# Performance work log

Hardware: AMD Instinct MI355X
Metric: run time of the kernel (lower is better)

## Reference

```python
import jax, jax.numpy as jnp
import numpy as np

B, SEQ, F = 256, 2048, 5
IN1, U1, U2 = SEQ * F, 32, 1
UNFOLDS = 6          # ODE solver unfolds per cell call
ELAPSED = 1.0        # elapsed time per call


def _cell_params(key, n_in, n_u):
    ks = jax.random.split(key, 9)
    U = lambda k, shp, lo, hi: jax.random.uniform(k, shp, jnp.float32, lo, hi)
    return dict(
        input_w=jnp.ones((n_in,), jnp.float32),
        input_b=jnp.zeros((n_in,), jnp.float32),
        smu=U(ks[0], (n_in, n_u), 0.3, 0.8),
        ssig=U(ks[1], (n_in, n_u), 3.0, 8.0),
        sW=U(ks[2], (n_in, n_u), 0.001, 1.0),
        serev=2.0 * jax.random.bernoulli(ks[3], 0.5, (n_in, n_u)).astype(jnp.float32) - 1.0,
        mu=U(ks[4], (n_u, n_u), 0.3, 0.8),
        sig=U(ks[5], (n_u, n_u), 3.0, 8.0),
        W=U(ks[6], (n_u, n_u), 0.001, 1.0),
        erev=2.0 * jax.random.bernoulli(ks[7], 0.5, (n_u, n_u)).astype(jnp.float32) - 1.0,
        gleak=jnp.ones((n_u,), jnp.float32),
        vleak=U(ks[8], (n_u,), -0.2, 0.2),
        cm=0.5 * jnp.ones((n_u,), jnp.float32),
    )


def setup_inputs() -> dict:
    key = jax.random.key(0)
    kx, ka, kb = jax.random.split(key, 3)
    inp = {"x": jax.random.normal(kx, (B, SEQ, F), jnp.float32)}
    for pfx, k, n_in, n_u in (("a_", ka, IN1, U1), ("b_", kb, U1, U2)):
        for name, v in _cell_params(k, n_in, n_u).items():
            inp[pfx + name] = v
    return inp


def _ltc(x, iw, ib, smu, ssig, sW, serev, mu, sig, W, erev, gleak, vleak, cm):
    # x: [B, n_in]; input affine mapping
    x = x * iw + ib
    # sensory synapse activations: [B, n_in, n_u]
    sact = sW * jax.nn.sigmoid((x[:, :, None] - smu) * ssig)
    w_num_s = jnp.einsum('biu,iu->bu', sact, serev)   # reversal-weighted sum
    w_den_s = jnp.sum(sact, axis=1)
    cm_t = cm / (ELAPSED / UNFOLDS)                   # [n_u]
    v0 = jnp.zeros((x.shape[0], cm.shape[0]), x.dtype)

    def body(v, _):
        # recurrent synapses: presyn axis 1, postsyn axis 2 -> [B, n_u, n_u]
        wact = W * jax.nn.sigmoid((v[:, :, None] - mu) * sig)
        num = cm_t * v + gleak * vleak + jnp.einsum('bij,ij->bj', wact, erev) + w_num_s
        den = cm_t + gleak + jnp.sum(wact, axis=1) + w_den_s
        return num / den, None

    v, _ = jax.lax.scan(body, v0, None, length=UNFOLDS)
    return v


def reference(x,
              a_input_w, a_input_b, a_smu, a_ssig, a_sW, a_serev,
              a_mu, a_sig, a_W, a_erev, a_gleak, a_vleak, a_cm,
              b_input_w, b_input_b, b_smu, b_ssig, b_sW, b_serev,
              b_mu, b_sig, b_W, b_erev, b_gleak, b_vleak, b_cm):
    bsz = x.shape[0]
    xb = x.reshape(bsz, -1)  # [B, seq*5]
    h = _ltc(xb, a_input_w, a_input_b, a_smu, a_ssig, a_sW, a_serev,
             a_mu, a_sig, a_W, a_erev, a_gleak, a_vleak, a_cm)     # [B, 32]
    h2 = _ltc(h, b_input_w, b_input_b, b_smu, b_ssig, b_sW, b_serev,
              b_mu, b_sig, b_W, b_erev, b_gleak, b_vleak, b_cm)    # [B, 1]
    return jax.nn.sigmoid(h2).reshape(bsz)
```

## Files before the change

### kernel.cpp

```cpp
#include <hip/hip_runtime.h>

#define BATCH 256
#define IN1   10240
#define NU    32
#define NB    32
#define BGROUPS (BATCH / NB)
#define LOG2E 1.4426950408889634f

__global__ __launch_bounds__(256) void ltc_sensory_partial(
    const float* __restrict__ x,
    const float* __restrict__ iw, const float* __restrict__ ibias,
    const float* __restrict__ smu, const float* __restrict__ ssig,
    const float* __restrict__ sW, const float* __restrict__ serev,
    float* __restrict__ pnum, float* __restrict__ pden,
    int stripe)
{
    const int tid = threadIdx.x;
    const int u   = tid & 31;
    const int il  = tid >> 5;
    const int w   = tid >> 6;
    const int bg  = blockIdx.x;
    const int is  = blockIdx.y;
    const int b0  = bg * NB;
    const int ibase = is * stripe;
    const int iend  = (ibase + stripe < IN1) ? (ibase + stripe) : IN1;

    float accn[NB], accd[NB];
#pragma unroll
    for (int n = 0; n < NB; ++n) { accn[n] = 0.f; accd[n] = 0.f; }

    for (int i = ibase + il; i < iend; i += 8) {
        const int pi = i * NU + u;
        float A = ssig[pi] * LOG2E;
        const float C = (smu[pi] - ibias[i]) * A;
        A *= iw[i];
        const float sw  = sW[pi];
        const float swe = sw * serev[pi];
        const float* xp = x + i;
#pragma unroll
        for (int n = 0; n < NB; ++n) {
            const float xv = xp[(size_t)(b0 + n) * IN1];
            const float e  = __builtin_amdgcn_exp2f(C - xv * A);
            const float r  = __builtin_amdgcn_rcpf(1.0f + e);
            accd[n] = fmaf(sw,  r, accd[n]);
            accn[n] = fmaf(swe, r, accn[n]);
        }
    }

    __shared__ float wred[4][NB][NU][2];
#pragma unroll
    for (int n = 0; n < NB; ++n) {
        float vn = accn[n] + __shfl_xor(accn[n], 32, 64);
        float vd = accd[n] + __shfl_xor(accd[n], 32, 64);
        if ((tid & 63) < 32) {
            wred[w][n][u][0] = vn;
            wred[w][n][u][1] = vd;
        }
    }
    __syncthreads();
    for (int p = tid; p < NB * NU; p += 256) {
        const int n = p >> 5, uu = p & 31;
        const float sn = wred[0][n][uu][0] + wred[1][n][uu][0]
                       + wred[2][n][uu][0] + wred[3][n][uu][0];
        const float sd = wred[0][n][uu][1] + wred[1][n][uu][1]
                       + wred[2][n][uu][1] + wred[3][n][uu][1];
        const size_t gi = ((size_t)is * BATCH + (b0 + n)) * NU + uu;
        pnum[gi] = sn;
        pden[gi] = sd;
    }
}

__global__ __launch_bounds__(256) void ltc_unfold(
    const float* __restrict__ pnum, const float* __restrict__ pden, int nsplit,
    const float* __restrict__ amu, const float* __restrict__ asig,
    const float* __restrict__ aW,  const float* __restrict__ aerev,
    const float* __restrict__ agleak, const float* __restrict__ avleak,
    const float* __restrict__ acm,
    const float* __restrict__ b_iw, const float* __restrict__ b_ib,
    const float* __restrict__ b_smu, const float* __restrict__ b_ssig,
    const float* __restrict__ b_sW,  const float* __restrict__ b_serev,
    const float* __restrict__ b_mu,  const float* __restrict__ b_sig,
    const float* __restrict__ b_W,   const float* __restrict__ b_erev,
    const float* __restrict__ b_gleak, const float* __restrict__ b_vleak,
    const float* __restrict__ b_cm,
    float* __restrict__ out)
{
    const int tid = threadIdx.x;
    const int b   = blockIdx.x;
    const int u   = tid & 31;
    const int sl  = tid >> 5;

    __shared__ float sred[8][NU][2];
    __shared__ float pAp[NU*NU], pCp[NU*NU];
    __shared__ float pW[NU*NU],  pWE[NU*NU];

    for (int p = tid; p < NU * NU; p += 256) {
        const float sg = asig[p] * LOG2E;
        pAp[p] = sg;
        pCp[p] = amu[p] * sg;
        const float w = aW[p];
        pW[p]  = w;
        pWE[p] = w * aerev[p];
    }

    float sn = 0.f, sd = 0.f;
    for (int s = sl; s < nsplit; s += 8) {
        const size_t gi = ((size_t)s * BATCH + b) * NU + u;
        sn += pnum[gi];
        sd += pden[gi];
    }
    sred[sl][u][0] = sn;
    sred[sl][u][1] = sd;
    __syncthreads();

    if (tid >= 32) return;

    float Sn = 0.f, Sd = 0.f;
#pragma unroll
    for (int s2 = 0; s2 < 8; ++s2) {
        Sn += sred[s2][u][0];
        Sd += sred[s2][u][1];
    }

    const float cmt = acm[u] * 6.0f;
    const float gl  = agleak[u];
    const float gv  = gl * avleak[u];

    float v = 0.f;
    for (int k = 0; k < 6; ++k) {
        float rn = 0.f, rd = 0.f;
#pragma unroll
        for (int j = 0; j < NU; ++j) {
            const float vj = __shfl(v, j, 32);
            const int pi = j * NU + u;
            const float e = __builtin_amdgcn_exp2f(pCp[pi] - vj * pAp[pi]);
            const float r = __builtin_amdgcn_rcpf(1.0f + e);
            rn = fmaf(pWE[pi], r, rn);
            rd = fmaf(pW[pi],  r, rd);
        }
        const float num = cmt * v + gv + rn + Sn;
        const float den = cmt + gl + rd + Sd;
        v = num / den;
    }

    const float x2 = v * b_iw[u] + b_ib[u];
    const float e2 = __builtin_amdgcn_exp2f((b_smu[u] - x2) * b_ssig[u] * LOG2E);
    const float s2v = b_sW[u] * __builtin_amdgcn_rcpf(1.0f + e2);
    float wn = s2v * b_serev[u];
    float wd = s2v;
#pragma unroll
    for (int m = 16; m >= 1; m >>= 1) {
        wn += __shfl_xor(wn, m, 32);
        wd += __shfl_xor(wd, m, 32);
    }

    const float bcmt = b_cm[0] * 6.0f;
    const float bgl  = b_gleak[0];
    const float bgv  = bgl * b_vleak[0];
    const float bmu  = b_mu[0], bsig = b_sig[0], bW = b_W[0], berev = b_erev[0];
    float v2 = 0.f;
#pragma unroll
    for (int k = 0; k < 6; ++k) {
        const float ee = __builtin_amdgcn_exp2f((bmu - v2) * bsig * LOG2E);
        const float ws = bW * __builtin_amdgcn_rcpf(1.0f + ee);
        const float num = bcmt * v2 + bgv + ws * berev + wn;
        const float den = bcmt + bgl + ws + wd;
        v2 = num / den;
    }

    if (u == 0)
        out[b] = 1.0f / (1.0f + __builtin_amdgcn_exp2f(-v2 * LOG2E));
}

extern "C" void kernel_launch(void* const* d_in, const int* in_sizes, int n_in,
                              void* d_out, int out_size, void* d_ws, size_t ws_size,
                              hipStream_t stream) {
    const float* x       = (const float*)d_in[0];
    const float* a_iw    = (const float*)d_in[1];
    const float* a_ib    = (const float*)d_in[2];
    const float* a_smu   = (const float*)d_in[3];
    const float* a_ssig  = (const float*)d_in[4];
    const float* a_sW    = (const float*)d_in[5];
    const float* a_serev = (const float*)d_in[6];
    const float* a_mu    = (const float*)d_in[7];
    const float* a_sig   = (const float*)d_in[8];
    const float* a_W     = (const float*)d_in[9];
    const float* a_erev  = (const float*)d_in[10];
    const float* a_gleak = (const float*)d_in[11];
    const float* a_vleak = (const float*)d_in[12];
    const float* a_cm    = (const float*)d_in[13];
    const float* b_iw    = (const float*)d_in[14];
    const float* b_ib    = (const float*)d_in[15];
    const float* b_smu   = (const float*)d_in[16];
    const float* b_ssig  = (const float*)d_in[17];
    const float* b_sW    = (const float*)d_in[18];
    const float* b_serev = (const float*)d_in[19];
    const float* b_mu    = (const float*)d_in[20];
    const float* b_sig   = (const float*)d_in[21];
    const float* b_W     = (const float*)d_in[22];
    const float* b_erev  = (const float*)d_in[23];
    const float* b_gleak = (const float*)d_in[24];
    const float* b_vleak = (const float*)d_in[25];
    const float* b_cm    = (const float*)d_in[26];
    float* out = (float*)d_out;

    int splits = 128;
    while (splits > 1 &&
           (size_t)splits * BATCH * NU * 2 * sizeof(float) > ws_size)
        splits >>= 1;
    int stripe = (IN1 + splits - 1) / splits;
    stripe = (stripe + 7) & ~7;
    const int gy = (IN1 + stripe - 1) / stripe;

    float* pnum = (float*)d_ws;
    float* pden = pnum + (size_t)splits * BATCH * NU;

    dim3 grid1(BGROUPS, gy);
    ltc_sensory_partial<<<grid1, 256, 0, stream>>>(
        x, a_iw, a_ib, a_smu, a_ssig, a_sW, a_serev, pnum, pden, stripe);

    ltc_unfold<<<BATCH, 256, 0, stream>>>(
        pnum, pden, gy,
        a_mu, a_sig, a_W, a_erev, a_gleak, a_vleak, a_cm,
        b_iw, b_ib, b_smu, b_ssig, b_sW, b_serev,
        b_mu, b_sig, b_W, b_erev, b_gleak, b_vleak, b_cm,
        out);
}
```

Measured before the change: 50.67 us.

## Stage x tiles in LDS, interleave partials, split reduction from unfold kernel

The sensory kernel now loads an 80-column tile of x for its 32 batch rows into padded shared memory with coalesced float4 loads, replacing strided per-thread global reads with LDS reads. Partial num/den sums are written as interleaved float2. The cross-split reduction moves into its own kernel, and the unfold kernel handles 8 batch rows per block using all 8 wavefront slices instead of one. The cost is an extra kernel launch, more block-level synchronisation per tile, and shared memory reused through a union.

```diff
diff --git a/kernel.cpp b/kernel.cpp
--- a/kernel.cpp
+++ b/kernel.cpp
@@ -5,6 +5,8 @@
 #define NU    32
 #define NB    32
 #define BGROUPS (BATCH / NB)
+#define TILE_I 80
+#define XPAD   84
 #define LOG2E 1.4426950408889634f
 
 __global__ __launch_bounds__(256) void ltc_sensory_partial(
@@ -12,66 +14,119 @@
     const float* __restrict__ iw, const float* __restrict__ ibias,
     const float* __restrict__ smu, const float* __restrict__ ssig,
     const float* __restrict__ sW, const float* __restrict__ serev,
-    float* __restrict__ pnum, float* __restrict__ pden,
-    int stripe)
+    float2* __restrict__ part, int stripe)
 {
     const int tid = threadIdx.x;
     const int u   = tid & 31;
     const int il  = tid >> 5;
-    const int w   = tid >> 6;
-    const int bg  = blockIdx.x;
-    const int is  = blockIdx.y;
-    const int b0  = bg * NB;
-    const int ibase = is * stripe;
+    const int wv  = tid >> 6;
+    const int b0  = blockIdx.x * NB;
+    const int ibase = blockIdx.y * stripe;
     const int iend  = (ibase + stripe < IN1) ? (ibase + stripe) : IN1;
 
+    union SmemT {
+        float xL[NB][XPAD];
+        float wred[4][NB][NU][2];
+    };
+    __shared__ SmemT sm;
+
     float accn[NB], accd[NB];
 #pragma unroll
     for (int n = 0; n < NB; ++n) { accn[n] = 0.f; accd[n] = 0.f; }
 
-    for (int i = ibase + il; i < iend; i += 8) {
-        const int pi = i * NU + u;
-        float A = ssig[pi] * LOG2E;
-        const float C = (smu[pi] - ibias[i]) * A;
-        A *= iw[i];
-        const float sw  = sW[pi];
-        const float swe = sw * serev[pi];
-        const float* xp = x + i;
-#pragma unroll
-        for (int n = 0; n < NB; ++n) {
-            const float xv = xp[(size_t)(b0 + n) * IN1];
-            const float e  = __builtin_amdgcn_exp2f(C - xv * A);
-            const float r  = __builtin_amdgcn_rcpf(1.0f + e);
-            accd[n] = fmaf(sw,  r, accd[n]);
-            accn[n] = fmaf(swe, r, accn[n]);
-        }
-    }
-
-    __shared__ float wred[4][NB][NU][2];
+    const int lrow = tid >> 3;
+    const int lq   = tid & 7;
+
+    for (int cb = ibase; cb < iend; cb += TILE_I) {
+        const int cend = (cb + TILE_I < iend) ? (cb + TILE_I) : iend;
+        const int cw   = cend - cb;
+        __syncthreads();
+        const float* xrow = x + (size_t)(b0 + lrow) * IN1 + cb;
+        for (int c4 = lq; c4 * 4 < cw; c4 += 8) {
+            if (c4 * 4 + 3 < cw) {
+                const float4 v4 = *(const float4*)(xrow + c4 * 4);
+                *(float4*)&sm.xL[lrow][c4 * 4] = v4;
+            } else {
+                for (int t = c4 * 4; t < cw; ++t)
+                    sm.xL[lrow][t] = xrow[t];
+            }
+        }
+        __syncthreads();
+
+        for (int i = cb + il; i < cend; i += 8) {
+            const int pi = i * NU + u;
+            float A = ssig[pi] * LOG2E;
+            const float C = (smu[pi] - ibias[i]) * A;
+            A *= iw[i];
+            const float sw  = sW[pi];
+            const float swe = sw * serev[pi];
+            const float* xr = &sm.xL[0][0] + (i - cb);
+#pragma unroll
+            for (int n = 0; n < NB; ++n) {
+                const float xv = xr[n * XPAD];
+                const float e  = __builtin_amdgcn_exp2f(C - xv * A);
+                const float r  = __builtin_amdgcn_rcpf(1.0f + e);
+                accd[n] = fmaf(sw,  r, accd[n]);
+                accn[n] = fmaf(swe, r, accn[n]);
+            }
+        }
+    }
+
+    __syncthreads();
 #pragma unroll
     for (int n = 0; n < NB; ++n) {
         float vn = accn[n] + __shfl_xor(accn[n], 32, 64);
         float vd = accd[n] + __shfl_xor(accd[n], 32, 64);
         if ((tid & 63) < 32) {
-            wred[w][n][u][0] = vn;
-            wred[w][n][u][1] = vd;
+            sm.wred[wv][n][u][0] = vn;
+            sm.wred[wv][n][u][1] = vd;
         }
     }
     __syncthreads();
     for (int p = tid; p < NB * NU; p += 256) {
         const int n = p >> 5, uu = p & 31;
-        const float sn = wred[0][n][uu][0] + wred[1][n][uu][0]
-                       + wred[2][n][uu][0] + wred[3][n][uu][0];
-        const float sd = wred[0][n][uu][1] + wred[1][n][uu][1]
-                       + wred[2][n][uu][1] + wred[3][n][uu][1];
-        const size_t gi = ((size_t)is * BATCH + (b0 + n)) * NU + uu;
-        pnum[gi] = sn;
-        pden[gi] = sd;
-    }
+        const float sn = sm.wred[0][n][uu][0] + sm.wred[1][n][uu][0]
+                       + sm.wred[2][n][uu][0] + sm.wred[3][n][uu][0];
+        const float sd = sm.wred[0][n][uu][1] + sm.wred[1][n][uu][1]
+                       + sm.wred[2][n][uu][1] + sm.wred[3][n][uu][1];
+        part[((size_t)blockIdx.y * BATCH + (b0 + n)) * NU + uu] =
+            make_float2(sn, sd);
+    }
+}
+
+__global__ __launch_bounds__(256) void ltc_reduce(
+    const float2* __restrict__ part, int nsplit, float2* __restrict__ S)
+{
+    const int tid = threadIdx.x;
+    const int b   = blockIdx.x;
+    const int u   = tid & 31;
+    const int sl  = tid >> 5;
+
+    __shared__ float sred[8][NU][2];
+
+    float sn = 0.f, sd = 0.f;
+#pragma unroll 4
+    for (int s = sl; s < nsplit; s += 8) {
+        const float2 p = part[((size_t)s * BATCH + b) * NU + u];
+        sn += p.x;
+        sd += p.y;
+    }
+    sred[sl][u][0] = sn;
+    sred[sl][u][1] = sd;
+    __syncthreads();
+
+    if (tid >= 32) return;
+    float Sn = 0.f, Sd = 0.f;
+#pragma unroll
+    for (int s2 = 0; s2 < 8; ++s2) {
+        Sn += sred[s2][u][0];
+        Sd += sred[s2][u][1];
+    }
+    S[(size_t)b * NU + u] = make_float2(Sn, Sd);
 }
 
 __global__ __launch_bounds__(256) void ltc_unfold(
-    const float* __restrict__ pnum, const float* __restrict__ pden, int nsplit,
+    const float2* __restrict__ S,
     const float* __restrict__ amu, const float* __restrict__ asig,
     const float* __restrict__ aW,  const float* __restrict__ aerev,
     const float* __restrict__ agleak, const float* __restrict__ avleak,
@@ -86,11 +141,10 @@
     float* __restrict__ out)
 {
     const int tid = threadIdx.x;
-    const int b   = blockIdx.x;
     const int u   = tid & 31;
-    const int sl  = tid >> 5;
-
-    __shared__ float sred[8][NU][2];
+    const int bl  = tid >> 5;
+    const int b   = blockIdx.x * 8 + bl;
+
     __shared__ float pAp[NU*NU], pCp[NU*NU];
     __shared__ float pW[NU*NU],  pWE[NU*NU];
 
@@ -102,25 +156,10 @@
         pW[p]  = w;
         pWE[p] = w * aerev[p];
     }
-
-    float sn = 0.f, sd = 0.f;
-    for (int s = sl; s < nsplit; s += 8) {
-        const size_t gi = ((size_t)s * BATCH + b) * NU + u;
-        sn += pnum[gi];
-        sd += pden[gi];
-    }
-    sred[sl][u][0] = sn;
-    sred[sl][u][1] = sd;
-    __syncthreads();
-
-    if (tid >= 32) return;
-
-    float Sn = 0.f, Sd = 0.f;
-#pragma unroll
-    for (int s2 = 0; s2 < 8; ++s2) {
-        Sn += sred[s2][u][0];
-        Sd += sred[s2][u][1];
-    }
+    __syncthreads();
+
+    const float2 Sv = S[(size_t)b * NU + u];
+    const float Sn = Sv.x, Sd = Sv.y;
 
     const float cmt = acm[u] * 6.0f;
     const float gl  = agleak[u];
@@ -143,8 +182,8 @@
         v = num / den;
     }
 
-    const float x2 = v * b_iw[u] + b_ib[u];
-    const float e2 = __builtin_amdgcn_exp2f((b_smu[u] - x2) * b_ssig[u] * LOG2E);
+    const float x2  = v * b_iw[u] + b_ib[u];
+    const float e2  = __builtin_amdgcn_exp2f((b_smu[u] - x2) * b_ssig[u] * LOG2E);
     const float s2v = b_sW[u] * __builtin_amdgcn_rcpf(1.0f + e2);
     float wn = s2v * b_serev[u];
     float wd = s2v;
@@ -206,21 +245,23 @@
 
     int splits = 128;
     while (splits > 1 &&
-           (size_t)splits * BATCH * NU * 2 * sizeof(float) > ws_size)
+           ((size_t)splits * BATCH * NU + BATCH * NU) * sizeof(float2) > ws_size)
         splits >>= 1;
     int stripe = (IN1 + splits - 1) / splits;
     stripe = (stripe + 7) & ~7;
     const int gy = (IN1 + stripe - 1) / stripe;
 
-    float* pnum = (float*)d_ws;
-    float* pden = pnum + (size_t)splits * BATCH * NU;
+    float2* part = (float2*)d_ws;
+    float2* S    = part + (size_t)splits * BATCH * NU;
 
     dim3 grid1(BGROUPS, gy);
     ltc_sensory_partial<<<grid1, 256, 0, stream>>>(
-        x, a_iw, a_ib, a_smu, a_ssig, a_sW, a_serev, pnum, pden, stripe);
-
-    ltc_unfold<<<BATCH, 256, 0, stream>>>(
-        pnum, pden, gy,
+        x, a_iw, a_ib, a_smu, a_ssig, a_sW, a_serev, part, stripe);
+
+    ltc_reduce<<<BATCH, 256, 0, stream>>>(part, gy, S);
+
+    ltc_unfold<<<BATCH / 8, 256, 0, stream>>>(
+        S,
         a_mu, a_sig, a_W, a_erev, a_gleak, a_vleak, a_cm,
         b_iw, b_ib, b_smu, b_ssig, b_sW, b_serev,
         b_mu, b_sig, b_W, b_erev, b_gleak, b_vleak, b_cm,
```

Result: no change. 49.91 us (-1.5%).
